# Performance work log

Hardware: AMD Instinct MI355X
Metric: run time of the kernel (lower is better)

Reference implementation:

```python
import jax, jax.numpy as jnp
import numpy as np

N_GRAPHS = 64
NEG_SLOPE = 0.2

def setup_inputs() -> dict:
    key = jax.random.key(0)
    ks = jax.random.split(key, 8)
    N, E, F_IN, H, C, OUT = 50000, 800000, 128, 4, 32, 2
    x = jax.random.normal(ks[0], (N, F_IN), dtype=jnp.float32)
    edge_index = jax.random.randint(ks[1], (2, E), 0, N, dtype=jnp.int64)
    batch = jnp.sort(jax.random.randint(ks[2], (N,), 0, N_GRAPHS, dtype=jnp.int64))
    s = 1.0 / np.sqrt(F_IN)
    W = jax.random.normal(ks[3], (F_IN, H * C), dtype=jnp.float32) * s
    att_src = jax.random.normal(ks[4], (H, C), dtype=jnp.float32) * (1.0 / np.sqrt(C))
    att_dst = jax.random.normal(ks[5], (H, C), dtype=jnp.float32) * (1.0 / np.sqrt(C))
    bias_gat = jnp.zeros((H * C,), dtype=jnp.float32)
    W_lin = jax.random.normal(ks[6], (H * C, OUT), dtype=jnp.float32) * (1.0 / np.sqrt(H * C))
    b_lin = jnp.zeros((OUT,), dtype=jnp.float32)
    return {"x": x, "edge_index": edge_index, "batch": batch, "W": W,
            "att_src": att_src, "att_dst": att_dst, "bias_gat": bias_gat,
            "W_lin": W_lin, "b_lin": b_lin}

def reference(x, edge_index, batch, W, att_src, att_dst, bias_gat, W_lin, b_lin):
    N = x.shape[0]
    H, C = att_src.shape
    # linear projection: [N, H, C]
    xp = (x @ W).reshape(N, H, C)
    # per-node attention logits [N, H]
    a_src = jnp.einsum('nhc,hc->nh', xp, att_src)
    a_dst = jnp.einsum('nhc,hc->nh', xp, att_dst)
    # add self loops (PyG GATConv default add_self_loops=True)
    loop = jnp.arange(N, dtype=edge_index.dtype)
    src = jnp.concatenate([edge_index[0], loop])
    dst = jnp.concatenate([edge_index[1], loop])
    # per-edge logits + leaky relu
    e = a_src[src] + a_dst[dst]                       # [E+N, H]
    e = jnp.where(e >= 0, e, NEG_SLOPE * e)
    # segment softmax over destination node
    emax = jax.ops.segment_max(e, dst, num_segments=N)
    emax = jnp.where(jnp.isfinite(emax), emax, 0.0)
    ee = jnp.exp(e - emax[dst])
    denom = jax.ops.segment_sum(ee, dst, num_segments=N)
    alpha = ee / jnp.maximum(denom[dst], 1e-16)       # [E+N, H]
    # scatter-add aggregation of weighted source features
    msg = alpha[:, :, None] * xp[src]                 # [E+N, H, C]
    out = jax.ops.segment_sum(msg, dst, num_segments=N)  # [N, H, C]
    out = out.reshape(N, H * C) + bias_gat
    out = jax.nn.relu(out)
    # global mean pool per graph
    pooled = jax.ops.segment_sum(out, batch, num_segments=N_GRAPHS)
    counts = jax.ops.segment_sum(jnp.ones((N,), out.dtype), batch, num_segments=N_GRAPHS)
    pooled = pooled / jnp.maximum(counts, 1.0)[:, None]
    return pooled @ W_lin + b_lin
```

## Files before the change

kernel.cpp:

```cpp
#include <hip/hip_runtime.h>
#include <hip/hip_bf16.h>

#define HEADS 4
#define CH    32
#define HC    128
#define FIN   128
#define NG    64
#define POOL_CHUNKS 8
#define CAP   64

typedef __bf16 bf16x8 __attribute__((ext_vector_type(8)));
typedef float  f32x4  __attribute__((ext_vector_type(4)));

__global__ void wtrans_kernel(const float* __restrict__ W,
                              __hip_bfloat16* __restrict__ WT) {
    int t = blockIdx.x * 256 + threadIdx.x;
    if (t < HC * FIN) {
        int n = t >> 7, k = t & 127;
        WT[n * FIN + k] = __float2bfloat16(W[k * HC + n]);
    }
}

__global__ __launch_bounds__(256) void proj_mfma_kernel(const float* __restrict__ x,
                                                        const __hip_bfloat16* __restrict__ WT,
                                                        const float* __restrict__ att_src,
                                                        const float* __restrict__ att_dst,
                                                        __hip_bfloat16* __restrict__ xb,
                                                        float* __restrict__ a_src,
                                                        float* __restrict__ a_dst,
                                                        int N) {
    __shared__ char Xl[64 * 256];
    __shared__ char Wl[128 * 256];
    int t = threadIdx.x;
    int base = blockIdx.x * 64;

    for (int v = t; v < 1024; v += 256) {
        int row = v >> 4, g = v & 15;
        int node = base + row;
        union { bf16x8 v8; uint4 u4; } tmp;
        if (node < N) {
            float4 f0 = *(const float4*)&x[(size_t)node * FIN + g * 8];
            float4 f1 = *(const float4*)&x[(size_t)node * FIN + g * 8 + 4];
            tmp.v8[0] = (__bf16)f0.x; tmp.v8[1] = (__bf16)f0.y;
            tmp.v8[2] = (__bf16)f0.z; tmp.v8[3] = (__bf16)f0.w;
            tmp.v8[4] = (__bf16)f1.x; tmp.v8[5] = (__bf16)f1.y;
            tmp.v8[6] = (__bf16)f1.z; tmp.v8[7] = (__bf16)f1.w;
        } else {
            tmp.u4 = make_uint4(0, 0, 0, 0);
        }
        int gs = g ^ (row & 7);
        *(uint4*)&Xl[row * 256 + gs * 16] = tmp.u4;
    }
    for (int v = t; v < 2048; v += 256) {
        int n = v >> 4, g = v & 15;
        uint4 u = *(const uint4*)&WT[n * FIN + g * 8];
        int gs = g ^ (n & 7);
        *(uint4*)&Wl[n * 256 + gs * 16] = u;
    }
    __syncthreads();

    int wv = t >> 6, lane = t & 63;
    int lr = lane & 15, lg = lane >> 4;
    f32x4 acc[8];
#pragma unroll
    for (int tt = 0; tt < 8; tt++) acc[tt] = (f32x4){0.f, 0.f, 0.f, 0.f};

#pragma unroll
    for (int kc = 0; kc < 4; kc++) {
        int rowl = wv * 16 + lr;
        int ga = (kc * 4 + lg) ^ (lr & 7);
        bf16x8 a = *(bf16x8*)&Xl[rowl * 256 + ga * 16];
#pragma unroll
        for (int tt = 0; tt < 8; tt++) {
            int nr = tt * 16 + lr;
            int gb = (kc * 4 + lg) ^ (lr & 7);
            bf16x8 b = *(bf16x8*)&Wl[nr * 256 + gb * 16];
            acc[tt] = __builtin_amdgcn_mfma_f32_16x16x32_bf16(a, b, acc[tt], 0, 0, 0);
        }
    }

    float ps[4][4];
    float pd[4][4];
#pragma unroll
    for (int r = 0; r < 4; r++)
#pragma unroll
        for (int h = 0; h < 4; h++) { ps[r][h] = 0.f; pd[r][h] = 0.f; }

#pragma unroll
    for (int tt = 0; tt < 8; tt++) {
        int h = tt >> 1;
        int c = (tt & 1) * 16 + lr;
        float sv = att_src[h * CH + c];
        float dv = att_dst[h * CH + c];
        int col = tt * 16 + lr;
#pragma unroll
        for (int r = 0; r < 4; r++) {
            int row = base + wv * 16 + lg * 4 + r;
            float v = acc[tt][r];
            if (row < N) xb[(size_t)row * HC + col] = __float2bfloat16(v);
            ps[r][h] += v * sv;
            pd[r][h] += v * dv;
        }
    }

    __syncthreads();
    float* ssrc = (float*)Wl;
    float* sdst = ((float*)Wl) + 64 * 68;
#pragma unroll
    for (int r = 0; r < 4; r++) {
        int rowl = wv * 16 + lg * 4 + r;
#pragma unroll
        for (int h = 0; h < 4; h++) {
            ssrc[rowl * 68 + lr * 4 + h] = ps[r][h];
            sdst[rowl * 68 + lr * 4 + h] = pd[r][h];
        }
    }
    __syncthreads();
    {
        int rowl = t >> 2, h = t & 3;
        int node = base + rowl;
        float ss = 0.f, sd = 0.f;
#pragma unroll
        for (int q = 0; q < 16; q++) {
            ss += ssrc[rowl * 68 + q * 4 + h];
            sd += sdst[rowl * 68 + q * 4 + h];
        }
        if (node < N) {
            a_src[node * 4 + h] = ss;
            a_dst[node * 4 + h] = sd;
        }
    }
}

__global__ __launch_bounds__(256) void csr_scatter(const int* __restrict__ esrc,
                                                   const int* __restrict__ edst,
                                                   int* __restrict__ cnt,
                                                   unsigned short* __restrict__ bucket,
                                                   int E, int EN) {
    int b = blockIdx.x * 1024 + threadIdx.x;
    int i0 = b, i1 = b + 256, i2 = b + 512, i3 = b + 768;
    int s0, d0, s1, d1, s2, d2, s3, d3;
    bool v0 = i0 < EN, v1 = i1 < EN, v2 = i2 < EN, v3 = i3 < EN;
    if (v0) { if (i0 < E) { s0 = esrc[i0]; d0 = edst[i0]; } else { s0 = d0 = i0 - E; } }
    if (v1) { if (i1 < E) { s1 = esrc[i1]; d1 = edst[i1]; } else { s1 = d1 = i1 - E; } }
    if (v2) { if (i2 < E) { s2 = esrc[i2]; d2 = edst[i2]; } else { s2 = d2 = i2 - E; } }
    if (v3) { if (i3 < E) { s3 = esrc[i3]; d3 = edst[i3]; } else { s3 = d3 = i3 - E; } }
    int p0, p1, p2, p3;
    if (v0) p0 = atomicAdd(&cnt[d0], 1);
    if (v1) p1 = atomicAdd(&cnt[d1], 1);
    if (v2) p2 = atomicAdd(&cnt[d2], 1);
    if (v3) p3 = atomicAdd(&cnt[d3], 1);
    if (v0 && p0 < CAP) bucket[(size_t)d0 * CAP + p0] = (unsigned short)s0;
    if (v1 && p1 < CAP) bucket[(size_t)d1 * CAP + p1] = (unsigned short)s1;
    if (v2 && p2 < CAP) bucket[(size_t)d2 * CAP + p2] = (unsigned short)s2;
    if (v3 && p3 < CAP) bucket[(size_t)d3 * CAP + p3] = (unsigned short)s3;
}

__global__ __launch_bounds__(256) void agg_wave_kernel(const int* __restrict__ cnt,
                                                       const unsigned short* __restrict__ bucket,
                                                       const float* __restrict__ a_src,
                                                       const float* __restrict__ a_dst,
                                                       const __hip_bfloat16* __restrict__ xb,
                                                       float* __restrict__ agg, int N) {
    __shared__ int   sid[4][CAP];
    __shared__ float sw[4][CAP * 4];
    int wv = threadIdx.x >> 6;
    int lane = threadIdx.x & 63;
    int d = blockIdx.x * 4 + wv;
    if (d >= N) return;
    int deg = min(cnt[d], CAP);
    const unsigned short* lst = bucket + (size_t)d * CAP;

    if (lane < deg) sid[wv][lane] = lst[lane];

    float adh = a_dst[d * 4 + (lane & 3)];
    float wpart = 0.f;
    for (int p = lane; p < deg * 4; p += 64) {
        int i = p >> 2;
        int s = sid[wv][i];
        float e = a_src[s * 4 + (lane & 3)] + adh;
        e = e >= 0.f ? e : 0.2f * e;
        float w = __expf(e);
        sw[wv][p] = w;
        wpart += w;
    }
#pragma unroll
    for (int off = 4; off < 64; off <<= 1) wpart += __shfl_xor(wpart, off, 64);
    float rdc = 1.0f / fmaxf(wpart, 1e-16f);
    int h = lane >> 4;
    float rd = __shfl(rdc, h, 64);

    int j0 = lane * 2;
    float n0 = 0.f, n1 = 0.f;
    int i = 0;
    for (; i + 4 <= deg; i += 4) {
        int s0 = sid[wv][i], s1 = sid[wv][i + 1];
        int s2 = sid[wv][i + 2], s3 = sid[wv][i + 3];
        unsigned u0 = *(const unsigned*)&xb[(size_t)s0 * HC + j0];
        unsigned u1 = *(const unsigned*)&xb[(size_t)s1 * HC + j0];
        unsigned u2 = *(const unsigned*)&xb[(size_t)s2 * HC + j0];
        unsigned u3 = *(const unsigned*)&xb[(size_t)s3 * HC + j0];
        float w0 = sw[wv][(i + 0) * 4 + h], w1 = sw[wv][(i + 1) * 4 + h];
        float w2 = sw[wv][(i + 2) * 4 + h], w3 = sw[wv][(i + 3) * 4 + h];
        n0 += w0 * __uint_as_float(u0 << 16) + w1 * __uint_as_float(u1 << 16)
            + w2 * __uint_as_float(u2 << 16) + w3 * __uint_as_float(u3 << 16);
        n1 += w0 * __uint_as_float(u0 & 0xffff0000u) + w1 * __uint_as_float(u1 & 0xffff0000u)
            + w2 * __uint_as_float(u2 & 0xffff0000u) + w3 * __uint_as_float(u3 & 0xffff0000u);
    }
    for (; i < deg; i++) {
        int s0 = sid[wv][i];
        unsigned u0 = *(const unsigned*)&xb[(size_t)s0 * HC + j0];
        float w0 = sw[wv][i * 4 + h];
        n0 += w0 * __uint_as_float(u0 << 16);
        n1 += w0 * __uint_as_float(u0 & 0xffff0000u);
    }
    float2 o = make_float2(n0 * rd, n1 * rd);
    *(float2*)&agg[(size_t)d * HC + j0] = o;
}

__global__ __launch_bounds__(256) void pool_kernel(const float* __restrict__ agg,
                                                   const float* __restrict__ bias,
                                                   const int* __restrict__ batch,
                                                   float* __restrict__ pooled,
                                                   float* __restrict__ counts, int N) {
    int g = blockIdx.x / POOL_CHUNKS;
    int chunk = blockIdx.x % POOL_CHUNKS;
    int t = threadIdx.x;

    int lo = 0, hi = N;
    while (lo < hi) { int mid = (lo + hi) >> 1; if (batch[mid] < g) lo = mid + 1; else hi = mid; }
    int gstart = lo;
    hi = N;
    while (lo < hi) { int mid = (lo + hi) >> 1; if (batch[mid] < g + 1) lo = mid + 1; else hi = mid; }
    int gend = lo;
    int cnt = gend - gstart;

    int per = (cnt + POOL_CHUNKS - 1) / POOL_CHUNKS;
    int cstart = gstart + chunk * per;
    int cend = min(cstart + per, gend);

    int col = t & 31;
    int row = t >> 5;
    float4 b4 = *(const float4*)&bias[col * 4];
    float4 acc = make_float4(0.f, 0.f, 0.f, 0.f);
    for (int n = cstart + row; n < cend; n += 8) {
        float4 v = *(const float4*)&agg[(size_t)n * HC + col * 4];
        acc.x += fmaxf(v.x + b4.x, 0.f);
        acc.y += fmaxf(v.y + b4.y, 0.f);
        acc.z += fmaxf(v.z + b4.z, 0.f);
        acc.w += fmaxf(v.w + b4.w, 0.f);
    }

    __shared__ float4 red[256];
    red[t] = acc;
    __syncthreads();
    if (t < 128) {
        red[t].x += red[t + 128].x; red[t].y += red[t + 128].y;
        red[t].z += red[t + 128].z; red[t].w += red[t + 128].w;
    }
    __syncthreads();
    if (t < 64) {
        red[t].x += red[t + 64].x; red[t].y += red[t + 64].y;
        red[t].z += red[t + 64].z; red[t].w += red[t + 64].w;
    }
    __syncthreads();
    if (t < 32) {
        float4 r = red[t];
        r.x += red[t + 32].x; r.y += red[t + 32].y;
        r.z += red[t + 32].z; r.w += red[t + 32].w;
        atomicAdd(&pooled[g * HC + t * 4 + 0], r.x);
        atomicAdd(&pooled[g * HC + t * 4 + 1], r.y);
        atomicAdd(&pooled[g * HC + t * 4 + 2], r.z);
        atomicAdd(&pooled[g * HC + t * 4 + 3], r.w);
    }
    if (t == 0 && chunk == 0) counts[g] = (float)cnt;
}

__global__ void final_kernel(const float* __restrict__ pooled,
                             const float* __restrict__ counts,
                             const float* __restrict__ W_lin,
                             const float* __restrict__ b_lin,
                             float* __restrict__ out) {
    int t = threadIdx.x;
    int g = t >> 1, o = t & 1;
    float cnt = fmaxf(counts[g], 1.f);
    float sum = 0.f;
#pragma unroll 8
    for (int k = 0; k < HC; k++) sum += pooled[g * HC + k] * W_lin[k * 2 + o];
    out[g * 2 + o] = sum / cnt + b_lin[o];
}

extern "C" void kernel_launch(void* const* d_in, const int* in_sizes, int n_in,
                              void* d_out, int out_size, void* d_ws, size_t ws_size,
                              hipStream_t stream) {
    const float* x       = (const float*)d_in[0];
    const int*   eidx    = (const int*)d_in[1];
    const int*   batch   = (const int*)d_in[2];
    const float* W       = (const float*)d_in[3];
    const float* att_src = (const float*)d_in[4];
    const float* att_dst = (const float*)d_in[5];
    const float* bias    = (const float*)d_in[6];
    const float* W_lin   = (const float*)d_in[7];
    const float* b_lin   = (const float*)d_in[8];
    float* out = (float*)d_out;

    int N  = in_sizes[0] / FIN;
    int E  = in_sizes[1] / 2;
    int EN = E + N;
    const int* esrc = eidx;
    const int* edst = eidx + E;

    char* wsb = (char*)d_ws;
    __hip_bfloat16* xb = (__hip_bfloat16*)wsb; wsb += (size_t)N * HC * 2;
    float* a_src  = (float*)wsb;          wsb += (size_t)N * 4 * 4;
    float* a_dst  = (float*)wsb;          wsb += (size_t)N * 4 * 4;
    float* agg    = (float*)wsb;          wsb += (size_t)N * HC * 4;
    float* pooled = (float*)wsb;          wsb += (size_t)NG * HC * 4;
    float* counts = (float*)wsb;          wsb += (size_t)NG * 4;
    int*   cnt    = (int*)wsb;            wsb += (size_t)N * 4;
    unsigned short* bucket = (unsigned short*)wsb; wsb += (size_t)N * CAP * 2;
    __hip_bfloat16* WT = (__hip_bfloat16*)wsb; wsb += (size_t)HC * FIN * 2;

    hipMemsetAsync(cnt, 0, (size_t)N * sizeof(int), stream);
    hipMemsetAsync(pooled, 0, (size_t)(NG * HC + NG) * sizeof(float), stream);

    wtrans_kernel<<<(HC * FIN + 255) / 256, 256, 0, stream>>>(W, WT);
    proj_mfma_kernel<<<(N + 63) / 64, 256, 0, stream>>>(x, WT, att_src, att_dst,
                                                        xb, a_src, a_dst, N);
    csr_scatter<<<(EN + 1023) / 1024, 256, 0, stream>>>(esrc, edst, cnt, bucket, E, EN);
    agg_wave_kernel<<<(N + 3) / 4, 256, 0, stream>>>(cnt, bucket, a_src, a_dst, xb, agg, N);
    pool_kernel<<<NG * POOL_CHUNKS, 256, 0, stream>>>(agg, bias, batch, pooled, counts, N);
    final_kernel<<<1, 128, 0, stream>>>(pooled, counts, W_lin, b_lin, out);
}
```

Baseline: 199.6 us.

## Double projection tile rows per block and reduce attention logits via shuffles

The projection kernel now processes 128 nodes per block, with each wave computing two 16-row MFMA tiles that reuse the same W fragment loads from LDS. The per-node attention logit sums are reduced with xor shuffles within 16-lane groups instead of an LDS staging buffer and two block barriers. This cuts LDS traffic for W and the synchronization overhead. In exchange it doubles per-block LDS and register use and halves the number of blocks, which may lower occupancy.

```diff
diff --git a/kernel.cpp b/kernel.cpp
--- a/kernel.cpp
+++ b/kernel.cpp
@@ -29,12 +29,12 @@
                                                         float* __restrict__ a_src,
                                                         float* __restrict__ a_dst,
                                                         int N) {
-    __shared__ char Xl[64 * 256];
+    __shared__ char Xl[128 * 256];
     __shared__ char Wl[128 * 256];
     int t = threadIdx.x;
-    int base = blockIdx.x * 64;
-
-    for (int v = t; v < 1024; v += 256) {
+    int base = blockIdx.x * 128;
+
+    for (int v = t; v < 2048; v += 256) {
         int row = v >> 4, g = v & 15;
         int node = base + row;
         union { bf16x8 v8; uint4 u4; } tmp;
@@ -61,73 +61,69 @@
 
     int wv = t >> 6, lane = t & 63;
     int lr = lane & 15, lg = lane >> 4;
-    f32x4 acc[8];
-#pragma unroll
-    for (int tt = 0; tt < 8; tt++) acc[tt] = (f32x4){0.f, 0.f, 0.f, 0.f};
+    f32x4 acc[2][8];
+#pragma unroll
+    for (int m = 0; m < 2; m++)
+#pragma unroll
+        for (int tt = 0; tt < 8; tt++) acc[m][tt] = (f32x4){0.f, 0.f, 0.f, 0.f};
 
 #pragma unroll
     for (int kc = 0; kc < 4; kc++) {
-        int rowl = wv * 16 + lr;
         int ga = (kc * 4 + lg) ^ (lr & 7);
-        bf16x8 a = *(bf16x8*)&Xl[rowl * 256 + ga * 16];
+        bf16x8 a0 = *(bf16x8*)&Xl[(wv * 32 + lr) * 256 + ga * 16];
+        bf16x8 a1 = *(bf16x8*)&Xl[(wv * 32 + 16 + lr) * 256 + ga * 16];
 #pragma unroll
         for (int tt = 0; tt < 8; tt++) {
             int nr = tt * 16 + lr;
             int gb = (kc * 4 + lg) ^ (lr & 7);
             bf16x8 b = *(bf16x8*)&Wl[nr * 256 + gb * 16];
-            acc[tt] = __builtin_amdgcn_mfma_f32_16x16x32_bf16(a, b, acc[tt], 0, 0, 0);
-        }
-    }
-
-    float ps[4][4];
-    float pd[4][4];
-#pragma unroll
-    for (int r = 0; r < 4; r++)
-#pragma unroll
-        for (int h = 0; h < 4; h++) { ps[r][h] = 0.f; pd[r][h] = 0.f; }
-
-#pragma unroll
-    for (int tt = 0; tt < 8; tt++) {
-        int h = tt >> 1;
-        int c = (tt & 1) * 16 + lr;
-        float sv = att_src[h * CH + c];
-        float dv = att_dst[h * CH + c];
-        int col = tt * 16 + lr;
-#pragma unroll
-        for (int r = 0; r < 4; r++) {
-            int row = base + wv * 16 + lg * 4 + r;
-            float v = acc[tt][r];
-            if (row < N) xb[(size_t)row * HC + col] = __float2bfloat16(v);
-            ps[r][h] += v * sv;
-            pd[r][h] += v * dv;
-        }
-    }
-
-    __syncthreads();
-    float* ssrc = (float*)Wl;
-    float* sdst = ((float*)Wl) + 64 * 68;
-#pragma unroll
-    for (int r = 0; r < 4; r++) {
-        int rowl = wv * 16 + lg * 4 + r;
-#pragma unroll
-        for (int h = 0; h < 4; h++) {
-            ssrc[rowl * 68 + lr * 4 + h] = ps[r][h];
-            sdst[rowl * 68 + lr * 4 + h] = pd[r][h];
-        }
-    }
-    __syncthreads();
-    {
-        int rowl = t >> 2, h = t & 3;
-        int node = base + rowl;
-        float ss = 0.f, sd = 0.f;
-#pragma unroll
-        for (int q = 0; q < 16; q++) {
-            ss += ssrc[rowl * 68 + q * 4 + h];
-            sd += sdst[rowl * 68 + q * 4 + h];
-        }
-        if (node < N) {
-            a_src[node * 4 + h] = ss;
-            a_dst[node * 4 + h] = sd;
+            acc[0][tt] = __builtin_amdgcn_mfma_f32_16x16x32_bf16(a0, b, acc[0][tt], 0, 0, 0);
+            acc[1][tt] = __builtin_amdgcn_mfma_f32_16x16x32_bf16(a1, b, acc[1][tt], 0, 0, 0);
+        }
+    }
+
+#pragma unroll
+    for (int m = 0; m < 2; m++) {
+        float ps[4][4], pd[4][4];
+#pragma unroll
+        for (int r = 0; r < 4; r++)
+#pragma unroll
+            for (int h = 0; h < 4; h++) { ps[r][h] = 0.f; pd[r][h] = 0.f; }
+
+        int rowbase = base + wv * 32 + m * 16 + lg * 4;
+#pragma unroll
+        for (int tt = 0; tt < 8; tt++) {
+            int h = tt >> 1;
+            int c = (tt & 1) * 16 + lr;
+            float sv = att_src[h * CH + c];
+            float dv = att_dst[h * CH + c];
+            int col = tt * 16 + lr;
+#pragma unroll
+            for (int r = 0; r < 4; r++) {
+                int row = rowbase + r;
+                float v = acc[m][tt][r];
+                if (row < N) xb[(size_t)row * HC + col] = __float2bfloat16(v);
+                ps[r][h] += v * sv;
+                pd[r][h] += v * dv;
+            }
+        }
+#pragma unroll
+        for (int mask = 1; mask < 16; mask <<= 1) {
+#pragma unroll
+            for (int r = 0; r < 4; r++)
+#pragma unroll
+                for (int h = 0; h < 4; h++) {
+                    ps[r][h] += __shfl_xor(ps[r][h], mask, 16);
+                    pd[r][h] += __shfl_xor(pd[r][h], mask, 16);
+                }
+        }
+        {
+            int r = lr >> 2, h = lr & 3;
+            int node = rowbase + r;
+            if (node < N) {
+                a_src[node * 4 + h] = ps[r][h];
+                a_dst[node * 4 + h] = pd[r][h];
+            }
         }
     }
 }
@@ -325,8 +321,8 @@
     hipMemsetAsync(pooled, 0, (size_t)(NG * HC + NG) * sizeof(float), stream);
 
     wtrans_kernel<<<(HC * FIN + 255) / 256, 256, 0, stream>>>(W, WT);
-    proj_mfma_kernel<<<(N + 63) / 64, 256, 0, stream>>>(x, WT, att_src, att_dst,
-                                                        xb, a_src, a_dst, N);
+    proj_mfma_kernel<<<(N + 127) / 128, 256, 0, stream>>>(x, WT, att_src, att_dst,
+                                                          xb, a_src, a_dst, N);
     csr_scatter<<<(EN + 1023) / 1024, 256, 0, stream>>>(esrc, edst, cnt, bucket, E, EN);
     agg_wave_kernel<<<(N + 3) / 4, 256, 0, stream>>>(cnt, bucket, a_src, a_dst, xb, agg, N);
     pool_kernel<<<NG * POOL_CHUNKS, 256, 0, stream>>>(agg, bias, batch, pooled, counts, N);
```

After: 231.6 us. +16.1%, slower.
